# Kernel tuning notes

Measured on AMD Instinct MI355X. Metric: run time of the kernel, lower is better.

The kernel has to match this reference:

```python
import jax, jax.numpy as jnp
import numpy as np

N_NODES = 100000
N_EDGES = 1600000
D_IN = 128
D_OUT = 128


def setup_inputs() -> dict:
    key = jax.random.key(0)
    k1, k2, k3 = jax.random.split(key, 3)
    x = jax.random.normal(k1, (N_NODES, D_IN), dtype=jnp.float32)
    edge_indices = jax.random.randint(k2, (2, N_EDGES), 0, N_NODES, dtype=jnp.int64)
    # nn.Linear(input_dim, output_dim, bias=False): weight shape [out, in]
    W = jax.random.normal(k3, (D_OUT, D_IN), dtype=jnp.float32) * (1.0 / np.sqrt(D_IN))
    return {"x": x, "edge_indices": edge_indices, "W": W}


def reference(x, edge_indices, W):
    N = x.shape[0]
    # add self loops (i, i) for every node, as in create_norm_adj_mat
    self_loops = jnp.arange(N, dtype=edge_indices.dtype)
    row = jnp.concatenate([edge_indices[0], self_loops])  # [E+N]
    col = jnp.concatenate([edge_indices[1], self_loops])  # [E+N]
    # degree from row indices (torch.bincount(edge_indices[0]))
    deg = jax.ops.segment_sum(jnp.ones_like(row, dtype=x.dtype), row, num_segments=N)
    deg_rsqrt = jax.lax.rsqrt(deg)  # every node has a self loop -> deg >= 1
    vals = deg_rsqrt[row] * deg_rsqrt[col]  # [E+N] edge weights
    # dense linear projection first (linear(x)), then sparse aggregation
    h = x @ W.T  # [N, D_OUT]
    # (norm_adj_mat @ h)[i] = sum over edges with row==i of vals * h[col]
    agg = jax.ops.segment_sum(vals[:, None] * h[col], row, num_segments=N)  # [N, D_OUT]
    return jax.nn.relu(agg)
```

## Files before the change

### kernel.cpp

```cpp
#include <hip/hip_runtime.h>
#include <hip/hip_bf16.h>

#define D 128
#define SH 8
#define BROWS 256
#define NBK_MAX 512
#define CT 8
#define KS 4

typedef __bf16   bf16x8 __attribute__((ext_vector_type(8)));
typedef float    f32x4  __attribute__((ext_vector_type(4)));
typedef _Float16 f16x2  __attribute__((ext_vector_type(2)));
typedef _Float16 f16x4  __attribute__((ext_vector_type(4)));
typedef _Float16 f16x8  __attribute__((ext_vector_type(8)));

__global__ __launch_bounds__(256) void k_zero(int* __restrict__ p, int n) {
    for (int i = blockIdx.x * blockDim.x + threadIdx.x; i < n; i += gridDim.x * blockDim.x)
        p[i] = 0;
}

__global__ __launch_bounds__(256) void k_bucket_count(const int* __restrict__ rows,
                                                      int* __restrict__ bcnt, int E, int NBK) {
    __shared__ int h[NBK_MAX];
    for (int i = threadIdx.x; i < NBK; i += 256) h[i] = 0;
    __syncthreads();
    for (int e = blockIdx.x * blockDim.x + threadIdx.x; e < E; e += gridDim.x * blockDim.x)
        atomicAdd(&h[rows[e] >> SH], 1);
    __syncthreads();
    for (int i = threadIdx.x; i < NBK; i += 256) {
        int v = h[i];
        if (v) atomicAdd(&bcnt[i], v);
    }
}

__global__ __launch_bounds__(512) void k_scan_buckets(const int* __restrict__ bcnt,
                                                      int* __restrict__ boff,
                                                      int* __restrict__ bcur,
                                                      int* __restrict__ row_start,
                                                      int NBK, int N, int E) {
    __shared__ int sd[512];
    int t = threadIdx.x;
    int own = (t < NBK) ? bcnt[t] : 0;
    sd[t] = own;
    __syncthreads();
    for (int off = 1; off < 512; off <<= 1) {
        int add = (t >= off) ? sd[t - off] : 0;
        __syncthreads();
        sd[t] += add;
        __syncthreads();
    }
    if (t < NBK) {
        int ex = sd[t] - own;
        boff[t] = ex;
        bcur[t] = ex;
    }
    if (t == 0) {
        boff[NBK] = E;
        row_start[N] = E;
    }
}

__global__ __launch_bounds__(256) void k_pairs(const int* __restrict__ rows,
                                               const int* __restrict__ cols,
                                               int* __restrict__ bcur,
                                               unsigned* __restrict__ pairs,
                                               int E, int NBK, int chunk) {
    __shared__ int h[NBK_MAX];
    int e0 = blockIdx.x * chunk;
    if (e0 >= E) return;
    int e1 = min(E, e0 + chunk);
    for (int i = threadIdx.x; i < NBK; i += 256) h[i] = 0;
    __syncthreads();
    for (int e = e0 + threadIdx.x; e < e1; e += 256)
        atomicAdd(&h[rows[e] >> SH], 1);
    __syncthreads();
    for (int b = threadIdx.x; b < NBK; b += 256) {
        int v = h[b];
        h[b] = v ? atomicAdd(&bcur[b], v) : 0;
    }
    __syncthreads();
    for (int e = e0 + threadIdx.x; e < e1; e += 256) {
        int r = rows[e];
        int b = r >> SH;
        int p = atomicAdd(&h[b], 1);
        pairs[p] = ((unsigned)(r & (BROWS - 1)) << 24) | (unsigned)cols[e];
    }
}

__global__ __launch_bounds__(256) void k_bucket_finish(const unsigned* __restrict__ pairs,
                                                       const int* __restrict__ boff,
                                                       int* __restrict__ row_start,
                                                       float* __restrict__ dr,
                                                       int* __restrict__ csr_col, int N) {
    __shared__ int h[BROWS];
    __shared__ int cur[BROWS];
    int b = blockIdx.x;
    int t = threadIdx.x;
    int lim = min(N - (b << SH), BROWS);
    h[t] = 0;
    __syncthreads();
    int p0 = boff[b], p1 = boff[b + 1];
    for (int p = p0 + t; p < p1; p += 256)
        atomicAdd(&h[pairs[p] >> 24], 1);
    __syncthreads();
    int own = h[t];
    cur[t] = own;
    __syncthreads();
    for (int off = 1; off < 256; off <<= 1) {
        int add = (t >= off) ? cur[t - off] : 0;
        __syncthreads();
        cur[t] += add;
        __syncthreads();
    }
    int rs = p0 + cur[t] - own;
    if (t < lim) {
        row_start[(b << SH) + t] = rs;
        dr[(b << SH) + t] = rsqrtf((float)(own + 1));
    }
    __syncthreads();
    cur[t] = rs;
    __syncthreads();
    for (int p = p0 + t; p < p1; p += 256) {
        unsigned v = pairs[p];
        int q = atomicAdd(&cur[v >> 24], 1);
        csr_col[q] = (int)(v & 0xFFFFFF);
    }
}

__global__ __launch_bounds__(256) void k_half_s(const float4* __restrict__ x4,
                                                const float* __restrict__ dr,
                                                f16x4* __restrict__ xh4, int n4) {
    for (int i = blockIdx.x * blockDim.x + threadIdx.x; i < n4; i += gridDim.x * blockDim.x) {
        float d = dr[i >> 5];
        float4 v = x4[i];
        xh4[i] = (f16x4){(_Float16)(v.x * d), (_Float16)(v.y * d),
                         (_Float16)(v.z * d), (_Float16)(v.w * d)};
    }
}

__global__ __launch_bounds__(256) void k_prepW(const float* __restrict__ W,
                                               f16x8* __restrict__ Whi) {
    for (int f = blockIdx.x * blockDim.x + threadIdx.x; f < CT * KS * 64;
         f += gridDim.x * blockDim.x) {
        int l  = f & 63;
        int ks = (f >> 6) & 3;
        int ct = f >> 8;
        int o  = ct * 16 + (l & 15);
        int k0 = ks * 32 + ((l >> 4) * 8);
        const float* src = &W[o * D + k0];
        f16x8 hi;
#pragma unroll
        for (int i = 0; i < 8; ++i) hi[i] = (_Float16)src[i];
        Whi[f] = hi;
    }
}

__global__ __launch_bounds__(256) void k_gather_s(const int* __restrict__ row_start,
                                                  const int* __restrict__ csr_col,
                                                  const _Float16* __restrict__ xh,
                                                  const float* __restrict__ dr,
                                                  _Float16* __restrict__ aggh, int N) {
    int lane = threadIdx.x & 63;
    int gw = (blockIdx.x * blockDim.x + threadIdx.x) >> 6;
    int nw = (gridDim.x * blockDim.x) >> 6;
    for (int r = gw; r < N; r += nw) {
        float drr = dr[r];
        int beg = row_start[r], end = row_start[r + 1];
        const f16x2 xs = *(const f16x2*)&xh[(size_t)r * D + lane * 2];
        float a0 = (float)xs[0], a1 = (float)xs[1];
        for (int cb = beg; cb < end; cb += 64) {
            int m = end - cb;
            if (m > 64) m = 64;
            int cidx = (lane < m) ? csr_col[cb + lane] : 0;
            int j = 0;
            for (; j + 8 <= m; j += 8) {
                int c0 = __shfl(cidx, j);
                int c1 = __shfl(cidx, j + 1);
                int c2 = __shfl(cidx, j + 2);
                int c3 = __shfl(cidx, j + 3);
                int c4 = __shfl(cidx, j + 4);
                int c5 = __shfl(cidx, j + 5);
                int c6 = __shfl(cidx, j + 6);
                int c7 = __shfl(cidx, j + 7);
                f16x2 p0 = *(const f16x2*)&xh[(size_t)c0 * D + lane * 2];
                f16x2 p1 = *(const f16x2*)&xh[(size_t)c1 * D + lane * 2];
                f16x2 p2 = *(const f16x2*)&xh[(size_t)c2 * D + lane * 2];
                f16x2 p3 = *(const f16x2*)&xh[(size_t)c3 * D + lane * 2];
                f16x2 p4 = *(const f16x2*)&xh[(size_t)c4 * D + lane * 2];
                f16x2 p5 = *(const f16x2*)&xh[(size_t)c5 * D + lane * 2];
                f16x2 p6 = *(const f16x2*)&xh[(size_t)c6 * D + lane * 2];
                f16x2 p7 = *(const f16x2*)&xh[(size_t)c7 * D + lane * 2];
                a0 += (float)p0[0] + (float)p1[0] + (float)p2[0] + (float)p3[0]
                    + (float)p4[0] + (float)p5[0] + (float)p6[0] + (float)p7[0];
                a1 += (float)p0[1] + (float)p1[1] + (float)p2[1] + (float)p3[1]
                    + (float)p4[1] + (float)p5[1] + (float)p6[1] + (float)p7[1];
            }
            for (; j < m; ++j) {
                int c = __shfl(cidx, j);
                f16x2 p = *(const f16x2*)&xh[(size_t)c * D + lane * 2];
                a0 += (float)p[0];
                a1 += (float)p[1];
            }
        }
        f16x2 o = {(_Float16)(drr * a0), (_Float16)(drr * a1)};
        *(f16x2*)&aggh[(size_t)r * 256 + lane * 2] = o;
    }
}

__global__ __launch_bounds__(256) void k_project_g(const f16x8* __restrict__ Whi,
                                                   float* __restrict__ out, int N) {
    const _Float16* ah = (const _Float16*)out;
    int lane = threadIdx.x & 63;
    int wib  = threadIdx.x >> 6;
    int gw   = blockIdx.x * 4 + wib;
    int nw   = gridDim.x * 4;
    int nt   = N >> 4;
    int arow  = lane & 15;
    int kbase = (lane >> 4) * 8;

    for (int t = gw; t < nt; t += nw) {
        int row = t * 16 + arow;
        f16x8 A[KS];
#pragma unroll
        for (int ks = 0; ks < KS; ++ks)
            A[ks] = *(const f16x8*)&ah[(size_t)row * 256 + ks * 32 + kbase];

        f32x4 acc[CT];
#pragma unroll
        for (int ct = 0; ct < CT; ++ct) acc[ct] = (f32x4){0.f, 0.f, 0.f, 0.f};
#pragma unroll
        for (int ks = 0; ks < KS; ++ks) {
#pragma unroll
            for (int ct = 0; ct < CT; ++ct) {
                f16x8 bh = Whi[(ct * KS + ks) * 64 + lane];
                acc[ct] = __builtin_amdgcn_mfma_f32_16x16x32_f16(A[ks], bh, acc[ct], 0, 0, 0);
            }
        }
        int orow = t * 16 + (lane >> 4) * 4;
        int ocol = lane & 15;
#pragma unroll
        for (int ct = 0; ct < CT; ++ct) {
#pragma unroll
            for (int reg = 0; reg < 4; ++reg) {
                out[(size_t)(orow + reg) * D + ct * 16 + ocol] = fmaxf(acc[ct][reg], 0.f);
            }
        }
    }
}

__global__ __launch_bounds__(256) void k_gather(const int* __restrict__ row_start,
                                                const int* __restrict__ csr_col,
                                                const float* __restrict__ x,
                                                const float* __restrict__ dr,
                                                float* __restrict__ out, int N) {
    int lane = threadIdx.x & 63;
    int gw = (blockIdx.x * blockDim.x + threadIdx.x) >> 6;
    int nw = (gridDim.x * blockDim.x) >> 6;
    for (int r = gw; r < N; r += nw) {
        float drr = dr[r];
        int beg = row_start[r], end = row_start[r + 1];
        const float2 xs = *(const float2*)&x[(size_t)r * D + lane * 2];
        float s = drr * drr;
        float a0 = s * xs.x, a1 = s * xs.y;
        for (int cb = beg; cb < end; cb += 64) {
            int m = end - cb;
            if (m > 64) m = 64;
            int   cidx = (lane < m) ? csr_col[cb + lane] : 0;
            float cdr  = (lane < m) ? dr[cidx] : 0.f;
            int j = 0;
            for (; j + 4 <= m; j += 4) {
                int c0 = __shfl(cidx, j);
                int c1 = __shfl(cidx, j + 1);
                int c2 = __shfl(cidx, j + 2);
                int c3 = __shfl(cidx, j + 3);
                float v0 = drr * __shfl(cdr, j);
                float v1 = drr * __shfl(cdr, j + 1);
                float v2 = drr * __shfl(cdr, j + 2);
                float v3 = drr * __shfl(cdr, j + 3);
                const float2 p0 = *(const float2*)&x[(size_t)c0 * D + lane * 2];
                const float2 p1 = *(const float2*)&x[(size_t)c1 * D + lane * 2];
                const float2 p2 = *(const float2*)&x[(size_t)c2 * D + lane * 2];
                const float2 p3 = *(const float2*)&x[(size_t)c3 * D + lane * 2];
                a0 = fmaf(v0, p0.x, a0); a1 = fmaf(v0, p0.y, a1);
                a0 = fmaf(v1, p1.x, a0); a1 = fmaf(v1, p1.y, a1);
                a0 = fmaf(v2, p2.x, a0); a1 = fmaf(v2, p2.y, a1);
                a0 = fmaf(v3, p3.x, a0); a1 = fmaf(v3, p3.y, a1);
            }
            for (; j < m; ++j) {
                int   c = __shfl(cidx, j);
                float v = drr * __shfl(cdr, j);
                const float2 p = *(const float2*)&x[(size_t)c * D + lane * 2];
                a0 = fmaf(v, p.x, a0);
                a1 = fmaf(v, p.y, a1);
            }
        }
        float2 o;
        o.x = a0;
        o.y = a1;
        *(float2*)&out[(size_t)r * D + lane * 2] = o;
    }
}

__global__ __launch_bounds__(256) void k_project_mfma(const float* __restrict__ W,
                                                      float* __restrict__ out, int N) {
    __shared__ bf16x8 Bhi[CT * KS * 64];
    __shared__ bf16x8 Blo[CT * KS * 64];
    for (int f = threadIdx.x; f < CT * KS * 64; f += 256) {
        int l  = f & 63;
        int ks = (f >> 6) & 3;
        int ct = f >> 8;
        int o  = ct * 16 + (l & 15);
        int k0 = ks * 32 + ((l >> 4) * 8);
        const float* src = &W[o * D + k0];
        bf16x8 hi, lo;
#pragma unroll
        for (int i = 0; i < 8; ++i) {
            float v  = src[i];
            __bf16 h = (__bf16)v;
            hi[i] = h;
            lo[i] = (__bf16)(v - (float)h);
        }
        Bhi[f] = hi;
        Blo[f] = lo;
    }
    __syncthreads();

    int lane = threadIdx.x & 63;
    int wib  = threadIdx.x >> 6;
    int gw   = blockIdx.x * 4 + wib;
    int nw   = gridDim.x * 4;
    int nt   = N >> 4;
    int arow  = lane & 15;
    int kbase = (lane >> 4) * 8;

    for (int t = gw; t < nt; t += nw) {
        int row = t * 16 + arow;
        const float* arp = &out[(size_t)row * D + kbase];
        bf16x8 Ahi[KS], Alo[KS];
#pragma unroll
        for (int ks = 0; ks < KS; ++ks) {
            float4 v0 = *(const float4*)&arp[ks * 32];
            float4 v1 = *(const float4*)&arp[ks * 32 + 4];
            float va[8] = {v0.x, v0.y, v0.z, v0.w, v1.x, v1.y, v1.z, v1.w};
            bf16x8 hi, lo;
#pragma unroll
            for (int i = 0; i < 8; ++i) {
                __bf16 h = (__bf16)va[i];
                hi[i] = h;
                lo[i] = (__bf16)(va[i] - (float)h);
            }
            Ahi[ks] = hi;
            Alo[ks] = lo;
        }
        f32x4 acc[CT];
#pragma unroll
        for (int ct = 0; ct < CT; ++ct) acc[ct] = (f32x4){0.f, 0.f, 0.f, 0.f};
#pragma unroll
        for (int ks = 0; ks < KS; ++ks) {
#pragma unroll
            for (int ct = 0; ct < CT; ++ct) {
                bf16x8 bh = Bhi[(ct * KS + ks) * 64 + lane];
                bf16x8 bl = Blo[(ct * KS + ks) * 64 + lane];
                acc[ct] = __builtin_amdgcn_mfma_f32_16x16x32_bf16(Ahi[ks], bh, acc[ct], 0, 0, 0);
                acc[ct] = __builtin_amdgcn_mfma_f32_16x16x32_bf16(Alo[ks], bh, acc[ct], 0, 0, 0);
                acc[ct] = __builtin_amdgcn_mfma_f32_16x16x32_bf16(Ahi[ks], bl, acc[ct], 0, 0, 0);
            }
        }
        int orow = t * 16 + (lane >> 4) * 4;
        int ocol = lane & 15;
#pragma unroll
        for (int ct = 0; ct < CT; ++ct) {
#pragma unroll
            for (int reg = 0; reg < 4; ++reg) {
                out[(size_t)(orow + reg) * D + ct * 16 + ocol] = fmaxf(acc[ct][reg], 0.f);
            }
        }
    }
}

__global__ __launch_bounds__(256) void k_init_deg(int* __restrict__ deg, int n) {
    for (int i = blockIdx.x * blockDim.x + threadIdx.x; i < n; i += gridDim.x * blockDim.x)
        deg[i] = 1;
}
__global__ __launch_bounds__(256) void k_count_atomic(const int* __restrict__ rows,
                                                      int* __restrict__ cnt, int E) {
    for (int e = blockIdx.x * blockDim.x + threadIdx.x; e < E; e += gridDim.x * blockDim.x)
        atomicAdd(&cnt[rows[e]], 1);
}
__global__ __launch_bounds__(256) void k_rsqrt(float* __restrict__ buf, int n) {
    const int* di = (const int*)buf;
    for (int i = blockIdx.x * blockDim.x + threadIdx.x; i < n; i += gridDim.x * blockDim.x) {
        int v = di[i];
        buf[i] = rsqrtf((float)v);
    }
}
__global__ __launch_bounds__(256) void k_init_out(const float4* __restrict__ x4,
                                                  const float* __restrict__ dr,
                                                  float4* __restrict__ out4, int n4) {
    for (int i = blockIdx.x * blockDim.x + threadIdx.x; i < n4; i += gridDim.x * blockDim.x) {
        float d = dr[i >> 5];
        float s = d * d;
        float4 v = x4[i];
        out4[i] = make_float4(v.x * s, v.y * s, v.z * s, v.w * s);
    }
}
__global__ __launch_bounds__(256) void k_edges(const int* __restrict__ rows,
                                               const int* __restrict__ cols,
                                               const float* __restrict__ x,
                                               const float* __restrict__ dr,
                                               float* __restrict__ out, int E) {
    int lane = threadIdx.x & 63;
    int wib  = threadIdx.x >> 6;
    int gw   = blockIdx.x * 4 + wib;
    int nw   = gridDim.x * 4;
    for (int e = gw; e < E; e += nw) {
        int r = rows[e];
        int c = cols[e];
        float val = dr[r] * dr[c];
        const float2 xv = *(const float2*)&x[(size_t)c * D + lane * 2];
        float* po = &out[(size_t)r * D + lane * 2];
        unsafeAtomicAdd(po,     val * xv.x);
        unsafeAtomicAdd(po + 1, val * xv.y);
    }
}

extern "C" void kernel_launch(void* const* d_in, const int* in_sizes, int n_in,
                              void* d_out, int out_size, void* d_ws, size_t ws_size,
                              hipStream_t stream) {
    const float* x   = (const float*)d_in[0];
    const int*   idx = (const int*)d_in[1];
    const float* W   = (const float*)d_in[2];
    float*       out = (float*)d_out;

    int N = in_sizes[0] / D;
    int E = in_sizes[1] / 2;
    const int* rows = idx;
    const int* cols = idx + E;

    int NBK = (N + BROWS - 1) >> SH;

    size_t off = 0;
    size_t o_pairs = off;  off += (size_t)E;
    size_t o_csr   = off;  off += (size_t)E;
    size_t o_rs    = off;  off += (size_t)N + 1;
    size_t o_dr    = off;  off += (size_t)N;
    size_t o_bcnt  = off;  off += (size_t)NBK;
    size_t o_boff  = off;  off += (size_t)NBK + 1;
    size_t o_bcur  = off;  off += (size_t)NBK;
    off = (off + 3) & ~(size_t)3;
    size_t need_mid = off * 4;
    size_t o_whi   = off;  off += (size_t)(CT * KS * 64) * 4;
    size_t o_xh    = off;  off += ((size_t)N * D) / 2;
    size_t need_full = off * 4;

    int* wsw = (int*)d_ws;
    bool shape_ok = (NBK <= NBK_MAX) && ((N & 15) == 0) && (N < (1 << 24));

    if (shape_ok && ws_size >= need_mid) {
        unsigned* pairs     = (unsigned*)(wsw + o_pairs);
        int*      csr_col   = wsw + o_csr;
        int*      row_start = wsw + o_rs;
        float*    dr        = (float*)(wsw + o_dr);
        int*      bcnt      = wsw + o_bcnt;
        int*      boff      = wsw + o_boff;
        int*      bcur      = wsw + o_bcur;

        const int CHUNK = 2048;
        k_zero<<<(NBK + 255) / 256, 256, 0, stream>>>(bcnt, NBK);
        k_bucket_count<<<512, 256, 0, stream>>>(rows, bcnt, E, NBK);
        k_scan_buckets<<<1, 512, 0, stream>>>(bcnt, boff, bcur, row_start, NBK, N, E);
        k_pairs<<<(E + CHUNK - 1) / CHUNK, 256, 0, stream>>>(rows, cols, bcur, pairs,
                                                             E, NBK, CHUNK);
        k_bucket_finish<<<NBK, 256, 0, stream>>>(pairs, boff, row_start, dr, csr_col, N);

        if (ws_size >= need_full) {
            f16x8*    Whi = (f16x8*)(wsw + o_whi);
            _Float16* xh  = (_Float16*)(wsw + o_xh);
            k_half_s<<<2048, 256, 0, stream>>>((const float4*)x, dr, (f16x4*)xh, N * (D / 4));
            k_prepW<<<8, 256, 0, stream>>>(W, Whi);
            _Float16* aggh = (_Float16*)out;
            k_gather_s<<<4096, 256, 0, stream>>>(row_start, csr_col, xh, dr, aggh, N);
            int nt = N >> 4;
            k_project_g<<<(nt + 3) / 4, 256, 0, stream>>>(Whi, out, N);
        } else {
            k_gather<<<4096, 256, 0, stream>>>(row_start, csr_col, x, dr, out, N);
            int nt = N >> 4;
            k_project_mfma<<<(nt + 3) / 4, 256, 0, stream>>>(W, out, N);
        }
    } else {
        int*   deg = (int*)d_ws;
        float* dr  = (float*)d_ws;
        k_init_deg<<<(N + 255) / 256, 256, 0, stream>>>(deg, N);
        k_count_atomic<<<2048, 256, 0, stream>>>(rows, deg, E);
        k_rsqrt<<<(N + 255) / 256, 256, 0, stream>>>(dr, N);
        int n4 = N * (D / 4);
        k_init_out<<<4096, 256, 0, stream>>>((const float4*)x, dr, (float4*)out, n4);
        k_edges<<<4096, 256, 0, stream>>>(rows, cols, x, dr, out, E);
        int nt = N >> 4;
        k_project_mfma<<<(nt + 3) / 4, 256, 0, stream>>>(W, out, N);
    }
}
```

Before: 193.9 us.

## Widen gather loads to 16-byte f16x8, halve bucket size, fuse prep kernels

The gather kernel now has each wavefront split into four edge slots of sixteen lanes. Each lane loads eight halves (16 bytes) per neighbor, and the partial sums are combined with cross-lane shuffles at the end. This targets the narrow 4-byte per-lane gathers that limit memory-level parallelism. Bucket size is also halved (128 rows, up to 1024 buckets) with a matching 1024-thread scan and 128-thread finish blocks. The x-halving and W-prep kernels are merged into one launch. The risks are more shuffle and reduction work and lower lane utilization on short rows.

```diff
diff --git a/kernel.cpp b/kernel.cpp
--- a/kernel.cpp
+++ b/kernel.cpp
@@ -2,9 +2,9 @@
 #include <hip/hip_bf16.h>
 
 #define D 128
-#define SH 8
-#define BROWS 256
-#define NBK_MAX 512
+#define SH 7
+#define BROWS 128
+#define NBK_MAX 1024
 #define CT 8
 #define KS 4
 
@@ -33,17 +33,17 @@
     }
 }
 
-__global__ __launch_bounds__(512) void k_scan_buckets(const int* __restrict__ bcnt,
-                                                      int* __restrict__ boff,
-                                                      int* __restrict__ bcur,
-                                                      int* __restrict__ row_start,
-                                                      int NBK, int N, int E) {
-    __shared__ int sd[512];
+__global__ __launch_bounds__(1024) void k_scan_buckets(const int* __restrict__ bcnt,
+                                                       int* __restrict__ boff,
+                                                       int* __restrict__ bcur,
+                                                       int* __restrict__ row_start,
+                                                       int NBK, int N, int E) {
+    __shared__ int sd[1024];
     int t = threadIdx.x;
     int own = (t < NBK) ? bcnt[t] : 0;
     sd[t] = own;
     __syncthreads();
-    for (int off = 1; off < 512; off <<= 1) {
+    for (int off = 1; off < 1024; off <<= 1) {
         int add = (t >= off) ? sd[t - off] : 0;
         __syncthreads();
         sd[t] += add;
@@ -87,7 +87,7 @@
     }
 }
 
-__global__ __launch_bounds__(256) void k_bucket_finish(const unsigned* __restrict__ pairs,
+__global__ __launch_bounds__(128) void k_bucket_finish(const unsigned* __restrict__ pairs,
                                                        const int* __restrict__ boff,
                                                        int* __restrict__ row_start,
                                                        float* __restrict__ dr,
@@ -100,13 +100,13 @@
     h[t] = 0;
     __syncthreads();
     int p0 = boff[b], p1 = boff[b + 1];
-    for (int p = p0 + t; p < p1; p += 256)
+    for (int p = p0 + t; p < p1; p += 128)
         atomicAdd(&h[pairs[p] >> 24], 1);
     __syncthreads();
     int own = h[t];
     cur[t] = own;
     __syncthreads();
-    for (int off = 1; off < 256; off <<= 1) {
+    for (int off = 1; off < 128; off <<= 1) {
         int add = (t >= off) ? cur[t - off] : 0;
         __syncthreads();
         cur[t] += add;
@@ -120,28 +120,20 @@
     __syncthreads();
     cur[t] = rs;
     __syncthreads();
-    for (int p = p0 + t; p < p1; p += 256) {
+    for (int p = p0 + t; p < p1; p += 128) {
         unsigned v = pairs[p];
         int q = atomicAdd(&cur[v >> 24], 1);
         csr_col[q] = (int)(v & 0xFFFFFF);
     }
 }
 
-__global__ __launch_bounds__(256) void k_half_s(const float4* __restrict__ x4,
-                                                const float* __restrict__ dr,
-                                                f16x4* __restrict__ xh4, int n4) {
-    for (int i = blockIdx.x * blockDim.x + threadIdx.x; i < n4; i += gridDim.x * blockDim.x) {
-        float d = dr[i >> 5];
-        float4 v = x4[i];
-        xh4[i] = (f16x4){(_Float16)(v.x * d), (_Float16)(v.y * d),
-                         (_Float16)(v.z * d), (_Float16)(v.w * d)};
-    }
-}
-
-__global__ __launch_bounds__(256) void k_prepW(const float* __restrict__ W,
-                                               f16x8* __restrict__ Whi) {
-    for (int f = blockIdx.x * blockDim.x + threadIdx.x; f < CT * KS * 64;
-         f += gridDim.x * blockDim.x) {
+__global__ __launch_bounds__(256) void k_prep(const float4* __restrict__ x4,
+                                              const float* __restrict__ dr,
+                                              f16x4* __restrict__ xh4, int n4,
+                                              const float* __restrict__ W,
+                                              f16x8* __restrict__ Whi) {
+    if (blockIdx.x < 8) {
+        int f = blockIdx.x * 256 + threadIdx.x;
         int l  = f & 63;
         int ks = (f >> 6) & 3;
         int ct = f >> 8;
@@ -153,57 +145,76 @@
         for (int i = 0; i < 8; ++i) hi[i] = (_Float16)src[i];
         Whi[f] = hi;
     }
-}
-
-__global__ __launch_bounds__(256) void k_gather_s(const int* __restrict__ row_start,
+    for (int i = blockIdx.x * blockDim.x + threadIdx.x; i < n4; i += gridDim.x * blockDim.x) {
+        float d = dr[i >> 5];
+        float4 v = x4[i];
+        xh4[i] = (f16x4){(_Float16)(v.x * d), (_Float16)(v.y * d),
+                         (_Float16)(v.z * d), (_Float16)(v.w * d)};
+    }
+}
+
+__global__ __launch_bounds__(256) void k_gather_w(const int* __restrict__ row_start,
                                                   const int* __restrict__ csr_col,
                                                   const _Float16* __restrict__ xh,
                                                   const float* __restrict__ dr,
                                                   _Float16* __restrict__ aggh, int N) {
-    int lane = threadIdx.x & 63;
+    int lane  = threadIdx.x & 63;
+    int eslot = lane >> 4;
+    int dbase = (lane & 15) * 8;
     int gw = (blockIdx.x * blockDim.x + threadIdx.x) >> 6;
     int nw = (gridDim.x * blockDim.x) >> 6;
     for (int r = gw; r < N; r += nw) {
+        int beg = row_start[r], end = row_start[r + 1];
         float drr = dr[r];
-        int beg = row_start[r], end = row_start[r + 1];
-        const f16x2 xs = *(const f16x2*)&xh[(size_t)r * D + lane * 2];
-        float a0 = (float)xs[0], a1 = (float)xs[1];
+        float acc[8];
+        if (eslot == 0) {
+            f16x8 xs = *(const f16x8*)&xh[(size_t)r * D + dbase];
+#pragma unroll
+            for (int i = 0; i < 8; ++i) acc[i] = (float)xs[i];
+        } else {
+#pragma unroll
+            for (int i = 0; i < 8; ++i) acc[i] = 0.f;
+        }
         for (int cb = beg; cb < end; cb += 64) {
             int m = end - cb;
             if (m > 64) m = 64;
             int cidx = (lane < m) ? csr_col[cb + lane] : 0;
-            int j = 0;
-            for (; j + 8 <= m; j += 8) {
-                int c0 = __shfl(cidx, j);
-                int c1 = __shfl(cidx, j + 1);
-                int c2 = __shfl(cidx, j + 2);
-                int c3 = __shfl(cidx, j + 3);
-                int c4 = __shfl(cidx, j + 4);
-                int c5 = __shfl(cidx, j + 5);
-                int c6 = __shfl(cidx, j + 6);
-                int c7 = __shfl(cidx, j + 7);
-                f16x2 p0 = *(const f16x2*)&xh[(size_t)c0 * D + lane * 2];
-                f16x2 p1 = *(const f16x2*)&xh[(size_t)c1 * D + lane * 2];
-                f16x2 p2 = *(const f16x2*)&xh[(size_t)c2 * D + lane * 2];
-                f16x2 p3 = *(const f16x2*)&xh[(size_t)c3 * D + lane * 2];
-                f16x2 p4 = *(const f16x2*)&xh[(size_t)c4 * D + lane * 2];
-                f16x2 p5 = *(const f16x2*)&xh[(size_t)c5 * D + lane * 2];
-                f16x2 p6 = *(const f16x2*)&xh[(size_t)c6 * D + lane * 2];
-                f16x2 p7 = *(const f16x2*)&xh[(size_t)c7 * D + lane * 2];
-                a0 += (float)p0[0] + (float)p1[0] + (float)p2[0] + (float)p3[0]
-                    + (float)p4[0] + (float)p5[0] + (float)p6[0] + (float)p7[0];
-                a1 += (float)p0[1] + (float)p1[1] + (float)p2[1] + (float)p3[1]
-                    + (float)p4[1] + (float)p5[1] + (float)p6[1] + (float)p7[1];
-            }
-            for (; j < m; ++j) {
-                int c = __shfl(cidx, j);
-                f16x2 p = *(const f16x2*)&xh[(size_t)c * D + lane * 2];
-                a0 += (float)p[0];
-                a1 += (float)p[1];
-            }
-        }
-        f16x2 o = {(_Float16)(drr * a0), (_Float16)(drr * a1)};
-        *(f16x2*)&aggh[(size_t)r * 256 + lane * 2] = o;
+            int g = 0;
+            for (; g + 16 <= m; g += 16) {
+                int c0 = __shfl(cidx, g + eslot);
+                int c1 = __shfl(cidx, g + 4 + eslot);
+                int c2 = __shfl(cidx, g + 8 + eslot);
+                int c3 = __shfl(cidx, g + 12 + eslot);
+                f16x8 p0 = *(const f16x8*)&xh[(size_t)c0 * D + dbase];
+                f16x8 p1 = *(const f16x8*)&xh[(size_t)c1 * D + dbase];
+                f16x8 p2 = *(const f16x8*)&xh[(size_t)c2 * D + dbase];
+                f16x8 p3 = *(const f16x8*)&xh[(size_t)c3 * D + dbase];
+#pragma unroll
+                for (int i = 0; i < 8; ++i)
+                    acc[i] += ((float)p0[i] + (float)p1[i]) + ((float)p2[i] + (float)p3[i]);
+            }
+            for (; g < m; g += 4) {
+                int srcl = g + eslot;
+                bool valid = srcl < m;
+                int c = __shfl(cidx, valid ? srcl : 0);
+                if (valid) {
+                    f16x8 pv = *(const f16x8*)&xh[(size_t)c * D + dbase];
+#pragma unroll
+                    for (int i = 0; i < 8; ++i) acc[i] += (float)pv[i];
+                }
+            }
+        }
+#pragma unroll
+        for (int i = 0; i < 8; ++i) {
+            acc[i] += __shfl_xor(acc[i], 16);
+            acc[i] += __shfl_xor(acc[i], 32);
+        }
+        if (lane < 16) {
+            f16x8 o;
+#pragma unroll
+            for (int i = 0; i < 8; ++i) o[i] = (_Float16)(drr * acc[i]);
+            *(f16x8*)&aggh[(size_t)r * 256 + dbase] = o;
+        }
     }
 }
 
@@ -468,18 +479,18 @@
         const int CHUNK = 2048;
         k_zero<<<(NBK + 255) / 256, 256, 0, stream>>>(bcnt, NBK);
         k_bucket_count<<<512, 256, 0, stream>>>(rows, bcnt, E, NBK);
-        k_scan_buckets<<<1, 512, 0, stream>>>(bcnt, boff, bcur, row_start, NBK, N, E);
+        k_scan_buckets<<<1, 1024, 0, stream>>>(bcnt, boff, bcur, row_start, NBK, N, E);
         k_pairs<<<(E + CHUNK - 1) / CHUNK, 256, 0, stream>>>(rows, cols, bcur, pairs,
                                                              E, NBK, CHUNK);
-        k_bucket_finish<<<NBK, 256, 0, stream>>>(pairs, boff, row_start, dr, csr_col, N);
+        k_bucket_finish<<<NBK, 128, 0, stream>>>(pairs, boff, row_start, dr, csr_col, N);
 
         if (ws_size >= need_full) {
             f16x8*    Whi = (f16x8*)(wsw + o_whi);
             _Float16* xh  = (_Float16*)(wsw + o_xh);
-            k_half_s<<<2048, 256, 0, stream>>>((const float4*)x, dr, (f16x4*)xh, N * (D / 4));
-            k_prepW<<<8, 256, 0, stream>>>(W, Whi);
+            k_prep<<<2048, 256, 0, stream>>>((const float4*)x, dr, (f16x4*)xh, N * (D / 4),
+                                             W, Whi);
             _Float16* aggh = (_Float16*)out;
-            k_gather_s<<<4096, 256, 0, stream>>>(row_start, csr_col, xh, dr, aggh, N);
+            k_gather_w<<<4096, 256, 0, stream>>>(row_start, csr_col, xh, dr, aggh, N);
             int nt = N >> 4;
             k_project_g<<<(nt + 3) / 4, 256, 0, stream>>>(Whi, out, N);
         } else {
```

After: 207.1 us. +6.8%, slower.
